# Kernel optimization log

Hardware: AMD Instinct MI355X
Metric: run time of the kernel (lower is better)

## Reference

```python
import jax, jax.numpy as jnp
import numpy as np


def setup_inputs() -> dict:
    key = jax.random.key(0)
    ks = jax.random.split(key, 8)
    B, K, L, D = 8, 8, 4096, 256
    S = 1024  # windowlen
    inp = {
        "input": jax.random.normal(ks[0], (B, K, L, D), dtype=jnp.float32),
        "event_time": jax.random.uniform(ks[1], (B, L), dtype=jnp.float32),
        "W1": jax.random.normal(ks[2], (D, 2 * D), dtype=jnp.float32) / np.sqrt(D),
        "b1": jnp.zeros((2 * D,), dtype=jnp.float32),
        "W2": jax.random.normal(ks[3], (2 * D, D), dtype=jnp.float32) / np.sqrt(2 * D),
        "b2": jnp.zeros((D,), dtype=jnp.float32),
        "W3": jax.random.normal(ks[4], (D, 1), dtype=jnp.float32) / np.sqrt(D),
        "windowlen": S,
    }
    return inp


def reference(input, event_time, W1, b1, W2, b2, W3, windowlen):
    B, K, L, D = input.shape
    S = windowlen
    idx = jnp.arange(0, 2 * S, 2)  # strided window indices, [S]
    x = input.reshape(B * K, L, D)  # (BK, L, D)
    x_s = x[:, idx, :]  # (BK, S, D) indexed gather

    # offset MLP: D -> 2D -> D -> 1 (dropout inactive at eval)
    h = jax.nn.relu(jnp.einsum('bsd,de->bse', x_s, W1) + b1)
    h = jax.nn.relu(jnp.einsum('bse,ed->bsd', h, W2) + b2)
    offset = jnp.einsum('bsd,do->bso', h, W3)  # (BK, S, 1)

    pos = idx.astype(input.dtype)[None, :, None] + offset  # (BK, S, 1)

    # mask: pos <= argmax(event_time) per batch
    limit = jax.lax.stop_gradient(jnp.argmax(event_time, axis=-1)).astype(input.dtype)  # (B,)
    mask = (pos.reshape(B, K, S) <= limit[:, None, None]).astype(jnp.float32)  # (B, K, S)

    # grid x = pos/(L-1)*2-1 un-normalizes back to exactly pos; y=0 hits row 0.
    p = pos[..., 0]  # (BK, S)
    x0 = jnp.floor(p)
    w = p - x0  # fractional weight (grad flows to p, floor is constant)
    i0 = x0.astype(jnp.int32)
    i1 = i0 + 1

    def gather(i):
        valid = ((i >= 0) & (i <= L - 1)).astype(x.dtype)[..., None]
        ic = jnp.clip(i, 0, L - 1)
        return jnp.take_along_axis(x, ic[..., None], axis=1) * valid  # (BK, S, D)

    out = (1.0 - w)[..., None] * gather(i0) + w[..., None] * gather(i1)
    out = out.reshape(B, K, S, D)
    return out, mask
```

## Files before the change

### kernel.cpp

```cpp
#include <hip/hip_runtime.h>
#include <math.h>

#define B_   8
#define K_   8
#define L_   4096
#define D_   256
#define H_   512
#define S_   1024
#define M_   65536
#define MAXF 4096

typedef _Float16 half8  __attribute__((ext_vector_type(8)));
typedef float    floatx4 __attribute__((ext_vector_type(4)));

#define WS_LIMIT   0
#define WS_COUNTER 64
#define WS_FLAGS   128
#define WS_W1T     65536
#define WS_W2T     (65536 + H_*D_*2)

__global__ __launch_bounds__(256) void prep_kernel(const float* __restrict__ et,
                                                   const float* __restrict__ W1,
                                                   const float* __restrict__ W2,
                                                   char* __restrict__ ws) {
  __shared__ float sv[256];
  __shared__ int   si[256];
  const int blk = blockIdx.x;
  const int t   = threadIdx.x;
  if (blk < 1024) {
    int e = blk * 256 + t;
    if (e < H_ * D_) {
      int n = e >> 8, k = e & 255;
      ((_Float16*)(ws + WS_W1T))[e] = (_Float16)W1[(size_t)k * H_ + n];
    } else {
      int e2 = e - H_ * D_;
      int n = e2 >> 9, k = e2 & 511;
      ((_Float16*)(ws + WS_W2T))[e2] = (_Float16)W2[(size_t)k * D_ + n];
    }
  } else if (blk < 1032) {
    int b = blk - 1024;
    const float* row = et + (size_t)b * L_;
    float best = -INFINITY; int bidx = 0;
    for (int i = t; i < L_; i += 256) {
      float v = row[i];
      if (v > best) { best = v; bidx = i; }
    }
    sv[t] = best; si[t] = bidx;
    __syncthreads();
    for (int sft = 128; sft > 0; sft >>= 1) {
      if (t < sft) {
        float v2 = sv[t + sft]; int i2 = si[t + sft];
        if (v2 > sv[t] || (v2 == sv[t] && i2 < si[t])) { sv[t] = v2; si[t] = i2; }
      }
      __syncthreads();
    }
    if (t == 0) ((float*)(ws + WS_LIMIT))[b] = (float)si[0];
  } else {
    if (t == 0) *(int*)(ws + WS_COUNTER) = 0;
  }
}

__global__ __launch_bounds__(256) void gemm1_kernel(
    const float* __restrict__ X, const char* __restrict__ ws,
    const float* __restrict__ b1, _Float16* __restrict__ h1out) {
  __shared__ _Float16 As[64 * 32];
  __shared__ _Float16 Bs[256 * 32];
  const _Float16* W1T = (const _Float16*)(ws + WS_W1T);

  const int t    = threadIdx.x;
  const int blk  = blockIdx.x;
  const int n0b  = (blk & 1) * 256;
  const int m0   = (blk >> 1) * 64;
  const int w    = t >> 6, lane = t & 63;
  const int lr   = lane & 15, quad = lane >> 4;
  const int rowoff = (w & 1) * 32, coloff = (w >> 1) * 128;

  floatx4 acc[2][8] = {};

  const int r = t >> 2, q = t & 3;
  const int m  = m0 + r;
  const int bk = m >> 10, s = m & 1023;
  const float* xrow = X + ((size_t)bk * L_ + 2 * s) * D_;

  for (int k0 = 0; k0 < D_; k0 += 32) {
    __syncthreads();
    {
      float4 v0 = *(const float4*)(xrow + k0 + q * 8);
      float4 v1 = *(const float4*)(xrow + k0 + q * 8 + 4);
      half8 h;
      h[0]=(_Float16)v0.x; h[1]=(_Float16)v0.y; h[2]=(_Float16)v0.z; h[3]=(_Float16)v0.w;
      h[4]=(_Float16)v1.x; h[5]=(_Float16)v1.y; h[6]=(_Float16)v1.z; h[7]=(_Float16)v1.w;
      *(half8*)(&As[r * 32 + q * 8]) = h;
    }
    {
      #pragma unroll
      for (int c = 0; c < 4; ++c) {
        int n = w * 64 + c * 16 + (lane >> 2);
        *(uint4*)((char*)Bs + n * 64 + (lane & 3) * 16) =
            *(const uint4*)(W1T + (size_t)(n0b + n) * D_ + k0 + (lane & 3) * 8);
      }
    }
    __syncthreads();
    half8 af[2], bf[8];
    #pragma unroll
    for (int mt = 0; mt < 2; ++mt)
      af[mt] = *(const half8*)&As[(rowoff + mt * 16 + lr) * 32 + quad * 8];
    #pragma unroll
    for (int nt = 0; nt < 8; ++nt)
      bf[nt] = *(const half8*)&Bs[(coloff + nt * 16 + lr) * 32 + quad * 8];
    #pragma unroll
    for (int mt = 0; mt < 2; ++mt)
      #pragma unroll
      for (int nt = 0; nt < 8; ++nt)
        acc[mt][nt] = __builtin_amdgcn_mfma_f32_16x16x32_f16(af[mt], bf[nt], acc[mt][nt], 0, 0, 0);
  }

  #pragma unroll
  for (int nt = 0; nt < 8; ++nt) {
    int col = n0b + coloff + nt * 16 + lr;
    float bias = b1[col];
    #pragma unroll
    for (int mt = 0; mt < 2; ++mt) {
      int rowb = m0 + rowoff + mt * 16 + quad * 4;
      #pragma unroll
      for (int rg = 0; rg < 4; ++rg) {
        float v = acc[mt][nt][rg] + bias;
        h1out[(size_t)(rowb + rg) * H_ + col] = (_Float16)(v > 0.f ? v : 0.f);
      }
    }
  }
}

__global__ __launch_bounds__(256) void gemm2_kernel(
    const float* __restrict__ X, char* __restrict__ ws,
    const float* __restrict__ b2, const float* __restrict__ W3,
    float* out, float* maskv) {
  __shared__ _Float16 As[64 * 32];
  __shared__ _Float16 Bs[256 * 32];
  __shared__ float psum[2][64];
  __shared__ float posl[64];
  const _Float16* W2T    = (const _Float16*)(ws + WS_W2T);
  const float*    limitf = (const float*)(ws + WS_LIMIT);
  int*            counter = (int*)(ws + WS_COUNTER);
  int*            flags   = (int*)(ws + WS_FLAGS);
  const _Float16* h1 = (const _Float16*)out;

  const int t    = threadIdx.x;
  const int m0   = blockIdx.x * 64;
  const int w    = t >> 6, lane = t & 63;
  const int lr   = lane & 15, quad = lane >> 4;
  const int rowoff = (w & 1) * 32, coloff = (w >> 1) * 128;

  floatx4 acc[2][8] = {};

  for (int k0 = 0; k0 < H_; k0 += 32) {
    __syncthreads();
    {
      int rr = t >> 2, qq = t & 3;
      *(uint4*)((char*)As + rr * 64 + qq * 16) =
          *(const uint4*)(h1 + (size_t)(m0 + rr) * H_ + k0 + qq * 8);
    }
    {
      #pragma unroll
      for (int c = 0; c < 4; ++c) {
        int n = w * 64 + c * 16 + (lane >> 2);
        *(uint4*)((char*)Bs + n * 64 + (lane & 3) * 16) =
            *(const uint4*)(W2T + (size_t)n * H_ + k0 + (lane & 3) * 8);
      }
    }
    __syncthreads();
    half8 af[2], bf[8];
    #pragma unroll
    for (int mt = 0; mt < 2; ++mt)
      af[mt] = *(const half8*)&As[(rowoff + mt * 16 + lr) * 32 + quad * 8];
    #pragma unroll
    for (int nt = 0; nt < 8; ++nt)
      bf[nt] = *(const half8*)&Bs[(coloff + nt * 16 + lr) * 32 + quad * 8];
    #pragma unroll
    for (int mt = 0; mt < 2; ++mt)
      #pragma unroll
      for (int nt = 0; nt < 8; ++nt)
        acc[mt][nt] = __builtin_amdgcn_mfma_f32_16x16x32_f16(af[mt], bf[nt], acc[mt][nt], 0, 0, 0);
  }

  float part[2][4] = {{0,0,0,0},{0,0,0,0}};
  #pragma unroll
  for (int nt = 0; nt < 8; ++nt) {
    int col = coloff + nt * 16 + lr;
    float bias = b2[col];
    float w3   = W3[col];
    #pragma unroll
    for (int mt = 0; mt < 2; ++mt)
      #pragma unroll
      for (int rg = 0; rg < 4; ++rg) {
        float h2 = acc[mt][nt][rg] + bias;
        h2 = h2 > 0.f ? h2 : 0.f;
        part[mt][rg] = fmaf(h2, w3, part[mt][rg]);
      }
  }
  #pragma unroll
  for (int mt = 0; mt < 2; ++mt)
    #pragma unroll
    for (int rg = 0; rg < 4; ++rg) {
      float p = part[mt][rg];
      p += __shfl_xor(p, 1, 64);
      p += __shfl_xor(p, 2, 64);
      p += __shfl_xor(p, 4, 64);
      p += __shfl_xor(p, 8, 64);
      if (lr == 0) psum[w >> 1][rowoff + mt * 16 + quad * 4 + rg] = p;
    }
  __syncthreads();
  if (t < 64) {
    int   mrow  = m0 + t;
    float off   = psum[0][t] + psum[1][t];
    int   s     = mrow & 1023;
    float pos   = (float)(2 * s) + off;
    float limit = limitf[mrow >> 13];
    maskv[mrow] = (pos <= limit) ? 1.f : 0.f;
    posl[t] = pos;
    float d = pos - limit;
    if (d < 0.5f && d > -0.5f) {
      int idx = atomicAdd(counter, 1);
      if (idx < MAXF) flags[idx] = mrow;
    }
  }
  __syncthreads();
  {
    const int c4 = t & 63, rg = t >> 6;
    const int bk = m0 >> 10;
    const float* xbase = X + (size_t)bk * (L_ * D_);
    #pragma unroll 4
    for (int rr = 0; rr < 16; ++rr) {
      int   rI = rg * 16 + rr;
      float p  = posl[rI];
      float x0f = floorf(p);
      float ww  = p - x0f;
      int i0 = (int)x0f, i1 = i0 + 1;
      float v0 = (i0 >= 0 && i0 < L_) ? (1.f - ww) : 0.f;
      float v1 = (i1 >= 0 && i1 < L_) ? ww : 0.f;
      int ic0 = min(max(i0, 0), L_ - 1), ic1 = min(max(i1, 0), L_ - 1);
      float4 g0 = *(const float4*)(xbase + (size_t)ic0 * D_ + c4 * 4);
      float4 g1 = *(const float4*)(xbase + (size_t)ic1 * D_ + c4 * 4);
      float4 o;
      o.x = v0 * g0.x + v1 * g1.x;
      o.y = v0 * g0.y + v1 * g1.y;
      o.z = v0 * g0.z + v1 * g1.z;
      o.w = v0 * g0.w + v1 * g1.w;
      *(float4*)(out + (size_t)(m0 + rI) * D_ + c4 * 4) = o;
    }
  }
}

__global__ __launch_bounds__(256) void fixup_kernel(
    const float* __restrict__ X,  const float* __restrict__ W1,
    const float* __restrict__ b1, const float* __restrict__ W2,
    const float* __restrict__ b2, const float* __restrict__ W3,
    const char* __restrict__ ws, float* __restrict__ maskv) {
  __shared__ float xs[256];
  __shared__ float h1s[512];
  __shared__ float red[4];
  const float* limitf  = (const float*)(ws + WS_LIMIT);
  const int*   counter = (const int*)(ws + WS_COUNTER);
  const int*   flags   = (const int*)(ws + WS_FLAGS);
  const int t = threadIdx.x;
  const int cnt = min(*counter, MAXF);
  for (int fi = blockIdx.x; fi < cnt; fi += 64) {
    int mrow = flags[fi];
    int bk = mrow >> 10, s = mrow & 1023;
    const float* xrow = X + ((size_t)bk * L_ + 2 * s) * D_;
    xs[t] = xrow[t];
    __syncthreads();
    #pragma unroll
    for (int jj = 0; jj < 2; ++jj) {
      int j = t + jj * 256;
      float a = b1[j];
      for (int d = 0; d < 256; ++d)
        a = fmaf(xs[d], W1[(size_t)d * H_ + j], a);
      h1s[j] = a > 0.f ? a : 0.f;
    }
    __syncthreads();
    {
      float a = b2[t];
      for (int e = 0; e < 512; ++e)
        a = fmaf(h1s[e], W2[(size_t)e * D_ + t], a);
      float h2 = a > 0.f ? a : 0.f;
      float pp = h2 * W3[t];
      #pragma unroll
      for (int o = 32; o >= 1; o >>= 1) pp += __shfl_xor(pp, o, 64);
      if ((t & 63) == 0) red[t >> 6] = pp;
    }
    __syncthreads();
    if (t == 0) {
      float off   = red[0] + red[1] + red[2] + red[3];
      float pos   = (float)(2 * s) + off;
      float limit = limitf[mrow >> 13];
      maskv[mrow] = (pos <= limit) ? 1.f : 0.f;
    }
    __syncthreads();
  }
}

extern "C" void kernel_launch(void* const* d_in, const int* in_sizes, int n_in,
                              void* d_out, int out_size, void* d_ws, size_t ws_size,
                              hipStream_t stream) {
  const float* X  = (const float*)d_in[0];
  const float* et = (const float*)d_in[1];
  const float* W1 = (const float*)d_in[2];
  const float* b1 = (const float*)d_in[3];
  const float* W2 = (const float*)d_in[4];
  const float* b2 = (const float*)d_in[5];
  const float* W3 = (const float*)d_in[6];
  float* out   = (float*)d_out;
  float* maskv = out + (size_t)M_ * D_;
  char*  ws    = (char*)d_ws;

  prep_kernel <<<1033, 256, 0, stream>>>(et, W1, W2, ws);
  gemm1_kernel<<<2048, 256, 0, stream>>>(X, ws, b1, (_Float16*)d_out);
  gemm2_kernel<<<1024, 256, 0, stream>>>(X, ws, b2, W3, out, maskv);
  fixup_kernel<<<64,   256, 0, stream>>>(X, W1, b1, W2, b2, W3, ws, maskv);
}
```

Measured before the change: 471.0 us.

## Fuse both MLP GEMMs into one kernel with LDS-resident hidden activations

Merges gemm1 and gemm2 into a single kernel. Each 64-row block stages its X tile in LDS as fp16, computes the hidden layer in two 256-column halves into a padded LDS buffer, then runs the second GEMM from that buffer. This removes the global round-trip of the fp16 h1 intermediate and one kernel launch. Weight tiles are double-buffered through registers with padded LDS strides to overlap loads and cut bank conflicts. In exchange, LDS use per block rises to roughly 120KB, so only one block fits per CU (launch_bounds 256,1), which may limit latency hiding.

```diff
diff --git a/kernel.cpp b/kernel.cpp
--- a/kernel.cpp
+++ b/kernel.cpp
@@ -18,6 +18,11 @@
 #define WS_FLAGS   128
 #define WS_W1T     65536
 #define WS_W2T     (65536 + H_*D_*2)
+
+#define XA_LD    264
+#define H1_LD    520
+#define BS_LD    40
+#define BS_ELEMS (256 * BS_LD)
 
 __global__ __launch_bounds__(256) void prep_kernel(const float* __restrict__ et,
                                                    const float* __restrict__ W1,
@@ -60,128 +65,128 @@
   }
 }
 
-__global__ __launch_bounds__(256) void gemm1_kernel(
-    const float* __restrict__ X, const char* __restrict__ ws,
-    const float* __restrict__ b1, _Float16* __restrict__ h1out) {
-  __shared__ _Float16 As[64 * 32];
-  __shared__ _Float16 Bs[256 * 32];
-  const _Float16* W1T = (const _Float16*)(ws + WS_W1T);
-
-  const int t    = threadIdx.x;
-  const int blk  = blockIdx.x;
-  const int n0b  = (blk & 1) * 256;
-  const int m0   = (blk >> 1) * 64;
-  const int w    = t >> 6, lane = t & 63;
-  const int lr   = lane & 15, quad = lane >> 4;
+__device__ __forceinline__ void run_gemm(
+    const _Float16* __restrict__ Bglob, const int ldb, const int nsteps,
+    const _Float16* __restrict__ Alds, const int lda,
+    _Float16* __restrict__ Bs, const int t, floatx4 (&acc)[2][8])
+{
+  const int lane = t & 63, w = t >> 6;
+  const int lr = lane & 15, quad = lane >> 4;
   const int rowoff = (w & 1) * 32, coloff = (w >> 1) * 128;
-
-  floatx4 acc[2][8] = {};
-
-  const int r = t >> 2, q = t & 3;
-  const int m  = m0 + r;
-  const int bk = m >> 10, s = m & 1023;
-  const float* xrow = X + ((size_t)bk * L_ + 2 * s) * D_;
-
-  for (int k0 = 0; k0 < D_; k0 += 32) {
-    __syncthreads();
-    {
-      float4 v0 = *(const float4*)(xrow + k0 + q * 8);
-      float4 v1 = *(const float4*)(xrow + k0 + q * 8 + 4);
-      half8 h;
-      h[0]=(_Float16)v0.x; h[1]=(_Float16)v0.y; h[2]=(_Float16)v0.z; h[3]=(_Float16)v0.w;
-      h[4]=(_Float16)v1.x; h[5]=(_Float16)v1.y; h[6]=(_Float16)v1.z; h[7]=(_Float16)v1.w;
-      *(half8*)(&As[r * 32 + q * 8]) = h;
-    }
-    {
-      #pragma unroll
-      for (int c = 0; c < 4; ++c) {
-        int n = w * 64 + c * 16 + (lane >> 2);
-        *(uint4*)((char*)Bs + n * 64 + (lane & 3) * 16) =
-            *(const uint4*)(W1T + (size_t)(n0b + n) * D_ + k0 + (lane & 3) * 8);
-      }
-    }
-    __syncthreads();
+  const int sr = lane >> 2, sk = lane & 3;
+  const int srow0 = w * 64 + sr;
+
+  uint4 breg[4];
+  #pragma unroll
+  for (int c = 0; c < 4; ++c)
+    breg[c] = *(const uint4*)(Bglob + (size_t)(srow0 + c * 16) * ldb + sk * 8);
+  #pragma unroll
+  for (int c = 0; c < 4; ++c)
+    *(uint4*)((char*)Bs + (srow0 + c * 16) * (BS_LD * 2) + sk * 16) = breg[c];
+  __syncthreads();
+
+  for (int ks = 0; ks < nsteps; ++ks) {
+    const _Float16* Bcur = Bs + (ks & 1) * BS_ELEMS;
+    if (ks + 1 < nsteps) {
+      const _Float16* src = Bglob + (ks + 1) * 32 + sk * 8;
+      #pragma unroll
+      for (int c = 0; c < 4; ++c)
+        breg[c] = *(const uint4*)(src + (size_t)(srow0 + c * 16) * ldb);
+    }
     half8 af[2], bf[8];
     #pragma unroll
     for (int mt = 0; mt < 2; ++mt)
-      af[mt] = *(const half8*)&As[(rowoff + mt * 16 + lr) * 32 + quad * 8];
+      af[mt] = *(const half8*)(Alds + (rowoff + mt * 16 + lr) * lda + ks * 32 + quad * 8);
     #pragma unroll
     for (int nt = 0; nt < 8; ++nt)
-      bf[nt] = *(const half8*)&Bs[(coloff + nt * 16 + lr) * 32 + quad * 8];
+      bf[nt] = *(const half8*)(Bcur + (coloff + nt * 16 + lr) * BS_LD + quad * 8);
     #pragma unroll
     for (int mt = 0; mt < 2; ++mt)
       #pragma unroll
       for (int nt = 0; nt < 8; ++nt)
         acc[mt][nt] = __builtin_amdgcn_mfma_f32_16x16x32_f16(af[mt], bf[nt], acc[mt][nt], 0, 0, 0);
-  }
-
-  #pragma unroll
-  for (int nt = 0; nt < 8; ++nt) {
-    int col = n0b + coloff + nt * 16 + lr;
-    float bias = b1[col];
-    #pragma unroll
-    for (int mt = 0; mt < 2; ++mt) {
-      int rowb = m0 + rowoff + mt * 16 + quad * 4;
-      #pragma unroll
-      for (int rg = 0; rg < 4; ++rg) {
-        float v = acc[mt][nt][rg] + bias;
-        h1out[(size_t)(rowb + rg) * H_ + col] = (_Float16)(v > 0.f ? v : 0.f);
-      }
-    }
-  }
-}
-
-__global__ __launch_bounds__(256) void gemm2_kernel(
+    if (ks + 1 < nsteps) {
+      _Float16* Bnxt = Bs + ((ks + 1) & 1) * BS_ELEMS;
+      #pragma unroll
+      for (int c = 0; c < 4; ++c)
+        *(uint4*)((char*)Bnxt + (srow0 + c * 16) * (BS_LD * 2) + sk * 16) = breg[c];
+    }
+    __syncthreads();
+  }
+}
+
+__global__ __launch_bounds__(256, 1) void fused_kernel(
     const float* __restrict__ X, char* __restrict__ ws,
-    const float* __restrict__ b2, const float* __restrict__ W3,
-    float* out, float* maskv) {
-  __shared__ _Float16 As[64 * 32];
-  __shared__ _Float16 Bs[256 * 32];
+    const float* __restrict__ b1, const float* __restrict__ b2,
+    const float* __restrict__ W3,
+    float* __restrict__ out, float* __restrict__ maskv) {
+  __shared__ __align__(16) _Float16 Xa[64 * XA_LD];
+  __shared__ __align__(16) _Float16 h1s[64 * H1_LD];
+  __shared__ __align__(16) _Float16 Bs[2 * BS_ELEMS];
   __shared__ float psum[2][64];
   __shared__ float posl[64];
+
+  const _Float16* W1T    = (const _Float16*)(ws + WS_W1T);
   const _Float16* W2T    = (const _Float16*)(ws + WS_W2T);
   const float*    limitf = (const float*)(ws + WS_LIMIT);
   int*            counter = (int*)(ws + WS_COUNTER);
   int*            flags   = (int*)(ws + WS_FLAGS);
-  const _Float16* h1 = (const _Float16*)out;
 
   const int t    = threadIdx.x;
   const int m0   = blockIdx.x * 64;
-  const int w    = t >> 6, lane = t & 63;
+  const int lane = t & 63, w = t >> 6;
   const int lr   = lane & 15, quad = lane >> 4;
   const int rowoff = (w & 1) * 32, coloff = (w >> 1) * 128;
-
-  floatx4 acc[2][8] = {};
-
-  for (int k0 = 0; k0 < H_; k0 += 32) {
-    __syncthreads();
-    {
-      int rr = t >> 2, qq = t & 3;
-      *(uint4*)((char*)As + rr * 64 + qq * 16) =
-          *(const uint4*)(h1 + (size_t)(m0 + rr) * H_ + k0 + qq * 8);
-    }
-    {
-      #pragma unroll
-      for (int c = 0; c < 4; ++c) {
-        int n = w * 64 + c * 16 + (lane >> 2);
-        *(uint4*)((char*)Bs + n * 64 + (lane & 3) * 16) =
-            *(const uint4*)(W2T + (size_t)n * H_ + k0 + (lane & 3) * 8);
+  const int bk   = m0 >> 10;
+
+  {
+    const int r = t >> 2, q = t & 3;
+    const int s = (m0 + r) & 1023;
+    const float* xrow = X + ((size_t)bk * L_ + 2 * s) * D_ + q * 64;
+    _Float16* dst = Xa + r * XA_LD + q * 64;
+    #pragma unroll
+    for (int i = 0; i < 8; ++i) {
+      float4 v0 = *(const float4*)(xrow + i * 8);
+      float4 v1 = *(const float4*)(xrow + i * 8 + 4);
+      half8 h;
+      h[0]=(_Float16)v0.x; h[1]=(_Float16)v0.y; h[2]=(_Float16)v0.z; h[3]=(_Float16)v0.w;
+      h[4]=(_Float16)v1.x; h[5]=(_Float16)v1.y; h[6]=(_Float16)v1.z; h[7]=(_Float16)v1.w;
+      *(half8*)(dst + i * 8) = h;
+    }
+  }
+
+  floatx4 acc[2][8];
+
+  #pragma unroll
+  for (int nh = 0; nh < 2; ++nh) {
+    #pragma unroll
+    for (int mt = 0; mt < 2; ++mt)
+      #pragma unroll
+      for (int nt = 0; nt < 8; ++nt)
+        acc[mt][nt] = (floatx4){0.f, 0.f, 0.f, 0.f};
+    run_gemm(W1T + (size_t)nh * 256 * D_, D_, 8, Xa, XA_LD, Bs, t, acc);
+    #pragma unroll
+    for (int nt = 0; nt < 8; ++nt) {
+      int col = nh * 256 + coloff + nt * 16 + lr;
+      float bias = b1[col];
+      #pragma unroll
+      for (int mt = 0; mt < 2; ++mt) {
+        int rowb = rowoff + mt * 16 + quad * 4;
+        #pragma unroll
+        for (int rg = 0; rg < 4; ++rg) {
+          float v = acc[mt][nt][rg] + bias;
+          h1s[(rowb + rg) * H1_LD + col] = (_Float16)(v > 0.f ? v : 0.f);
+        }
       }
     }
-    __syncthreads();
-    half8 af[2], bf[8];
-    #pragma unroll
-    for (int mt = 0; mt < 2; ++mt)
-      af[mt] = *(const half8*)&As[(rowoff + mt * 16 + lr) * 32 + quad * 8];
+  }
+
+  #pragma unroll
+  for (int mt = 0; mt < 2; ++mt)
     #pragma unroll
     for (int nt = 0; nt < 8; ++nt)
-      bf[nt] = *(const half8*)&Bs[(coloff + nt * 16 + lr) * 32 + quad * 8];
-    #pragma unroll
-    for (int mt = 0; mt < 2; ++mt)
-      #pragma unroll
-      for (int nt = 0; nt < 8; ++nt)
-        acc[mt][nt] = __builtin_amdgcn_mfma_f32_16x16x32_f16(af[mt], bf[nt], acc[mt][nt], 0, 0, 0);
-  }
+      acc[mt][nt] = (floatx4){0.f, 0.f, 0.f, 0.f};
+  run_gemm(W2T, H_, 16, h1s, H1_LD, Bs, t, acc);
 
   float part[2][4] = {{0,0,0,0},{0,0,0,0}};
   #pragma unroll
@@ -227,7 +232,6 @@
   __syncthreads();
   {
     const int c4 = t & 63, rg = t >> 6;
-    const int bk = m0 >> 10;
     const float* xbase = X + (size_t)bk * (L_ * D_);
     #pragma unroll 4
     for (int rr = 0; rr < 16; ++rr) {
@@ -257,7 +261,7 @@
     const float* __restrict__ b2, const float* __restrict__ W3,
     const char* __restrict__ ws, float* __restrict__ maskv) {
   __shared__ float xs[256];
-  __shared__ float h1s[512];
+  __shared__ float h1f[512];
   __shared__ float red[4];
   const float* limitf  = (const float*)(ws + WS_LIMIT);
   const int*   counter = (const int*)(ws + WS_COUNTER);
@@ -276,13 +280,13 @@
       float a = b1[j];
       for (int d = 0; d < 256; ++d)
         a = fmaf(xs[d], W1[(size_t)d * H_ + j], a);
-      h1s[j] = a > 0.f ? a : 0.f;
+      h1f[j] = a > 0.f ? a : 0.f;
     }
     __syncthreads();
     {
       float a = b2[t];
       for (int e = 0; e < 512; ++e)
-        a = fmaf(h1s[e], W2[(size_t)e * D_ + t], a);
+        a = fmaf(h1f[e], W2[(size_t)e * D_ + t], a);
       float h2 = a > 0.f ? a : 0.f;
       float pp = h2 * W3[t];
       #pragma unroll
@@ -315,7 +319,6 @@
   char*  ws    = (char*)d_ws;
 
   prep_kernel <<<1033, 256, 0, stream>>>(et, W1, W2, ws);
-  gemm1_kernel<<<2048, 256, 0, stream>>>(X, ws, b1, (_Float16*)d_out);
-  gemm2_kernel<<<1024, 256, 0, stream>>>(X, ws, b2, W3, out, maskv);
+  fused_kernel<<<1024, 256, 0, stream>>>(X, ws, b1, b2, W3, out, maskv);
   fixup_kernel<<<64,   256, 0, stream>>>(X, W1, b1, W2, b2, W3, ws, maskv);
 }
```

After: 482.3 us. 1.02x slower.
